# Performance work log

Hardware: AMD Instinct MI355X
Metric: run time of the kernel (lower is better)

Reference implementation:

```python
import jax, jax.numpy as jnp
import numpy as np

B, D_IN, D_OUT, N_CTRL = 8192, 512, 512, 8

def setup_inputs() -> dict:
    key = jax.random.key(0)
    k1, k2, k3, k4 = jax.random.split(key, 4)
    inputs = jax.random.normal(k1, (B, D_IN), dtype=jnp.float32)
    # routing weights: positive soft blend coefficients, normalized per sample
    raw = jax.random.uniform(k2, (B, N_CTRL), dtype=jnp.float32)
    weights = raw / jnp.sum(raw, axis=-1, keepdims=True)
    w = jax.random.normal(k3, (N_CTRL, D_IN, D_OUT), dtype=jnp.float32) * 0.05
    b = jax.random.normal(k4, (N_CTRL, D_OUT), dtype=jnp.float32) * 0.05
    return {"inputs": inputs, "weights": weights, "w": w, "b": b}

def reference(inputs, weights, w, b):
    # Original math: w_p = einsum('ji,imk->jmk', weights, w)  [B, D_IN, D_OUT]
    #                out = squeeze(inputs[:, None, :] @ w_p) + weights @ b
    # Fused equivalent avoiding the [B, D_IN, D_OUT] intermediate:
    # run all n_control expert matmuls, then blend by routing weights.
    per_expert = jnp.einsum('bi,cio->cbo', inputs, w)       # [C, B, D_OUT]
    out = jnp.einsum('bc,cbo->bo', weights, per_expert)     # [B, D_OUT]
    out = out + weights @ b                                 # blended bias [B, D_OUT]
    return out
```

## Files before the change

kernel.cpp:

```cpp
#include <hip/hip_runtime.h>

#define B_   8192
#define DIN  512
#define DOUT 512
#define NC   8
#define NCD  (NC * DIN)
#define KSPL 4

typedef float  f32x4 __attribute__((ext_vector_type(4)));
typedef short  s16x8 __attribute__((ext_vector_type(8)));
typedef unsigned short u16x4 __attribute__((ext_vector_type(4)));
typedef unsigned int   u32x4 __attribute__((ext_vector_type(4)));

__device__ __forceinline__ unsigned short f2bf(float f) {
  unsigned u = __builtin_bit_cast(unsigned, f);
  u += 0x7fffu + ((u >> 16) & 1u);
  return (unsigned short)(u >> 16);
}
__device__ __forceinline__ float bf2f(unsigned short h) {
  unsigned u = ((unsigned)h) << 16;
  return __builtin_bit_cast(float, u);
}
__device__ __forceinline__ unsigned cvtpk(float lo, float hi) {
  unsigned r;
  asm("v_cvt_pk_bf16_f32 %0, %1, %2" : "=v"(r) : "v"(lo), "v"(hi));
  return r;
}
__device__ __forceinline__ void gl2lds16(const void* g, void* l) {
  __builtin_amdgcn_global_load_lds(
      (const __attribute__((address_space(1))) void*)g,
      (__attribute__((address_space(3))) void*)l, 16, 0, 0);
}

__global__ void pack_xw_k(const f32x4* __restrict__ x, u16x4* __restrict__ xb,
                          const float* __restrict__ w, unsigned short* __restrict__ Wt) {
  __shared__ float tile[64][65];
  const int tid = threadIdx.x;
  if (blockIdx.x < 4096) {
    int gid = blockIdx.x * 256 + tid;
    f32x4 v = x[gid];
    u16x4 o;
    o[0] = f2bf(v[0]); o[1] = f2bf(v[1]); o[2] = f2bf(v[2]); o[3] = f2bf(v[3]);
    xb[gid] = o;
    return;
  }
  const int idx = blockIdx.x - 4096;
  const int kt = idx & 63, nt = idx >> 6;
#pragma unroll
  for (int it = 0; it < 16; ++it) {
    int u = it * 256 + tid;
    int r = u >> 6, cc = u & 63;
    tile[r][cc] = w[(size_t)(kt * 64 + r) * DOUT + nt * 64 + cc];
  }
  __syncthreads();
#pragma unroll
  for (int it = 0; it < 16; ++it) {
    int u = it * 256 + tid;
    int rn = u >> 6, ck = u & 63;
    Wt[(size_t)(nt * 64 + rn) * NCD + kt * 64 + ck] = f2bf(tile[ck][rn]);
  }
}

__global__ __launch_bounds__(512, 2) void gemm_k(
    const unsigned short* __restrict__ xb,
    const unsigned short* __restrict__ Wt,
    const float* __restrict__ wt,
    unsigned short* __restrict__ part) {
  extern __shared__ char smem[];
  const int tid  = threadIdx.x;
  const int lane = tid & 63, wid = tid >> 6;
  const int wm = wid >> 2, wn = wid & 3;
  const int l15 = lane & 15, lhi = lane >> 4;

  const int n0   = blockIdx.x;
  const int by   = n0 >> 3;
  const int bx   = (n0 >> 2) & 1;
  const int ks   = n0 & 3;
  const int brow = by * 256, bcol = bx * 256;

  const int srow = tid >> 3, schunk = tid & 7;
  const int swz  = schunk ^ (srow & 7);
  const unsigned short* gA = xb + (size_t)(brow + srow) * DIN + schunk * 8;
  const unsigned short* gB = Wt + (size_t)(bcol + srow) * NCD + ks * 1024 + swz * 8;
  char* adst = smem + srow * 128 + swz * 16;

  const float* wtp = wt + (size_t)(brow + srow) * NC + ks * 2;
  const float wtv0_0 = wtp[0],            wtv1_0 = wtp[1];
  const float wtv0_1 = wtp[64 * NC],      wtv1_1 = wtp[64 * NC + 1];
  const float wtv0_2 = wtp[128 * NC],     wtv1_2 = wtp[128 * NC + 1];
  const float wtv0_3 = wtp[192 * NC],     wtv1_3 = wtp[192 * NC + 1];

  f32x4 acc[8][4] = {};
  s16x8 areg0, areg1, areg2, areg3;
  s16x8 a[8], b[4];
  const int x7    = l15 & 7;
  const int pc0   = (lhi ^ x7) * 16;
  const int pc1   = ((4 + lhi) ^ x7) * 16;
  const int abase = (wm * 128 + l15) * 128;
  const int bbase = 32768 + (wn * 64 + l15) * 128;

#define STAGE_B(kt, ob) {                                                    \
    const unsigned short* s_ = gB + (size_t)(kt) * 64;                       \
    char* l_ = smem + (ob) + 32768 + tid * 16;                               \
    gl2lds16(s_,                          l_);                               \
    gl2lds16(s_ + (size_t) 64 * NCD,      l_ + 8192);                        \
    gl2lds16(s_ + (size_t)128 * NCD,      l_ + 16384);                       \
    gl2lds16(s_ + (size_t)192 * NCD,      l_ + 24576); }
#define LOAD_AREGS(kt) {                                                     \
    const unsigned short* s_ = gA + ((kt) & 7) * 64;                         \
    areg0 = *(const s16x8*)(s_);                                             \
    areg1 = *(const s16x8*)(s_ + (size_t) 64 * DIN);                         \
    areg2 = *(const s16x8*)(s_ + (size_t)128 * DIN);                         \
    areg3 = *(const s16x8*)(s_ + (size_t)192 * DIN); }
#define SCALE_STORE(AR, S, P, ob) {                                          \
    u32x4 v_;                                                                \
    v_[0] = cvtpk(bf2f((unsigned short)AR[0]) * (S),                         \
                  bf2f((unsigned short)AR[1]) * (S));                        \
    v_[1] = cvtpk(bf2f((unsigned short)AR[2]) * (S),                         \
                  bf2f((unsigned short)AR[3]) * (S));                        \
    v_[2] = cvtpk(bf2f((unsigned short)AR[4]) * (S),                         \
                  bf2f((unsigned short)AR[5]) * (S));                        \
    v_[3] = cvtpk(bf2f((unsigned short)AR[6]) * (S),                         \
                  bf2f((unsigned short)AR[7]) * (S));                        \
    *(u32x4*)(adst + (ob) + (P) * 8192) = v_; }
#define SCALE_WRITE_ALL(e_, ob) {                                            \
    SCALE_STORE(areg0, (e_) ? wtv1_0 : wtv0_0, 0, ob);                       \
    SCALE_STORE(areg1, (e_) ? wtv1_1 : wtv0_1, 1, ob);                       \
    SCALE_STORE(areg2, (e_) ? wtv1_2 : wtv0_2, 2, ob);                       \
    SCALE_STORE(areg3, (e_) ? wtv1_3 : wtv0_3, 3, ob); }
#define LOAD_FRAGS(cb, PC) {                                                 \
    const char* base_ = smem + (cb);                                         \
    _Pragma("unroll") for (int m = 0; m < 8; ++m)                            \
      a[m] = *(const s16x8*)(base_ + abase + m * 2048 + (PC));               \
    _Pragma("unroll") for (int n = 0; n < 4; ++n)                            \
      b[n] = *(const s16x8*)(base_ + bbase + n * 2048 + (PC)); }
#define MFMA_PAIR(N0, N1)                                                    \
    _Pragma("unroll") for (int m = 0; m < 8; ++m) {                          \
      acc[m][N0] = __builtin_amdgcn_mfma_f32_16x16x32_bf16(a[m], b[N0], acc[m][N0], 0, 0, 0); \
      acc[m][N1] = __builtin_amdgcn_mfma_f32_16x16x32_bf16(a[m], b[N1], acc[m][N1], 0, 0, 0); }
#define BAR()   __builtin_amdgcn_s_barrier()
#define PRIO1() __builtin_amdgcn_s_setprio(1)
#define PRIO0() __builtin_amdgcn_s_setprio(0)
#define PIN()   asm volatile("" ::: "memory")

  PIN();
  LOAD_AREGS(0);
  PIN();
  STAGE_B(0, 0);
  asm volatile("s_waitcnt vmcnt(4)" ::: "memory");
  SCALE_WRITE_ALL(0, 0);
  LOAD_AREGS(1);
  asm volatile("s_waitcnt lgkmcnt(0)" ::: "memory");

  for (int t = 0; t < 16; ++t) {
    const int cb = (t & 1) * 65536, ob = 65536 - cb;
    if (t < 15) {
      STAGE_B(t + 1, ob);
      asm volatile("s_waitcnt vmcnt(8)" ::: "memory");
    } else {
      asm volatile("s_waitcnt vmcnt(0)" ::: "memory");
    }
    BAR();
    LOAD_FRAGS(cb, pc0);
    PRIO1(); MFMA_PAIR(0, 1); MFMA_PAIR(2, 3); PRIO0();
    LOAD_FRAGS(cb, pc1);
    if (t < 15) {
      asm volatile("s_waitcnt vmcnt(4)" ::: "memory");
      const int e = ((t + 1) >> 3) & 1;
      SCALE_WRITE_ALL(e, ob);
      if (t < 14) LOAD_AREGS(t + 2);
    }
    asm volatile("s_waitcnt lgkmcnt(0)" ::: "memory");
    PRIO1(); MFMA_PAIR(0, 1); MFMA_PAIR(2, 3); PRIO0();
    BAR();
  }

  unsigned short* Cs = (unsigned short*)smem;
#pragma unroll
  for (int m = 0; m < 8; ++m)
#pragma unroll
    for (int n = 0; n < 4; ++n) {
      const int row = wm * 128 + m * 16 + lhi * 4;
      const int col = wn * 64 + n * 16 + l15;
      f32x4 v = acc[m][n];
#pragma unroll
      for (int j = 0; j < 4; ++j)
        Cs[(row + j) * 264 + col] = f2bf(v[j]);
    }
  __syncthreads();
  unsigned short* pc = part + (size_t)ks * (B_ * DOUT) + (size_t)brow * DOUT + bcol;
#pragma unroll
  for (int it = 0; it < 16; ++it) {
    const int u = it * 512 + tid;
    const int row = u >> 5, cu = (u & 31) * 8;
    f32x4 v = *(const f32x4*)(Cs + row * 264 + cu);
    *(f32x4*)(pc + (size_t)row * DOUT + cu) = v;
  }
#undef STAGE_B
#undef LOAD_AREGS
#undef SCALE_STORE
#undef SCALE_WRITE_ALL
#undef LOAD_FRAGS
#undef MFMA_PAIR
#undef BAR
#undef PRIO1
#undef PRIO0
#undef PIN
}

__global__ void reduce_k(const unsigned short* __restrict__ part,
                         const float* __restrict__ wt,
                         const float* __restrict__ bias,
                         float* __restrict__ out) {
  int gid = blockIdx.x * 256 + threadIdx.x;
  int b = gid >> 7;
  int o4 = (gid & 127) << 2;
  float w8[8];
  *(f32x4*)w8       = *(const f32x4*)(wt + (size_t)b * NC);
  *(f32x4*)(w8 + 4) = *(const f32x4*)(wt + (size_t)b * NC + 4);
  f32x4 acc = {0.f, 0.f, 0.f, 0.f};
  const size_t off = (size_t)b * DOUT + o4;
#pragma unroll
  for (int s = 0; s < KSPL; ++s) {
    u16x4 p = *(const u16x4*)(part + (size_t)s * (B_ * DOUT) + off);
#pragma unroll
    for (int i = 0; i < 4; ++i) acc[i] += bf2f(p[i]);
  }
#pragma unroll
  for (int cc = 0; cc < NC; ++cc) {
    f32x4 bi = *(const f32x4*)(bias + cc * DOUT + o4);
#pragma unroll
    for (int i = 0; i < 4; ++i) acc[i] += w8[cc] * bi[i];
  }
  *(f32x4*)(out + off) = acc;
}

__global__ void bias_only_k(const float* __restrict__ wt,
                            const float* __restrict__ bias,
                            float* __restrict__ out) {
  int gid = blockIdx.x * 256 + threadIdx.x;
  int b = gid >> 7;
  int o4 = (gid & 127) << 2;
  float w8[8];
  *(f32x4*)w8       = *(const f32x4*)(wt + (size_t)b * NC);
  *(f32x4*)(w8 + 4) = *(const f32x4*)(wt + (size_t)b * NC + 4);
  f32x4 acc = {0.f, 0.f, 0.f, 0.f};
#pragma unroll
  for (int cc = 0; cc < NC; ++cc) {
    f32x4 bi = *(const f32x4*)(bias + cc * DOUT + o4);
#pragma unroll
    for (int i = 0; i < 4; ++i) acc[i] += w8[cc] * bi[i];
  }
  *(f32x4*)(out + (size_t)b * DOUT + o4) = acc;
}

extern "C" void kernel_launch(void* const* d_in, const int* in_sizes, int n_in,
                              void* d_out, int out_size, void* d_ws, size_t ws_size,
                              hipStream_t stream) {
  const float *x = nullptr, *wtc = nullptr, *w = nullptr, *bias = nullptr;
  for (int i = 0; i < n_in; ++i) {
    switch (in_sizes[i]) {
      case B_ * DIN:        x    = (const float*)d_in[i]; break;
      case B_ * NC:         wtc  = (const float*)d_in[i]; break;
      case NC * DIN * DOUT: w    = (const float*)d_in[i]; break;
      case NC * DOUT:       bias = (const float*)d_in[i]; break;
    }
  }
  float* out = (float*)d_out;

  const size_t XB_ELEMS   = (size_t)B_ * DIN;
  const size_t WT_ELEMS   = (size_t)DOUT * NCD;
  const size_t PART_ELEMS = (size_t)KSPL * B_ * DOUT;
  const size_t need = (XB_ELEMS + WT_ELEMS + PART_ELEMS) * sizeof(unsigned short);

  if (ws_size < need) {
    bias_only_k<<<(B_ * DOUT / 4) / 256, 256, 0, stream>>>(wtc, bias, out);
    return;
  }

  unsigned short* xb   = (unsigned short*)d_ws;
  unsigned short* Wt   = xb + XB_ELEMS;
  unsigned short* part = Wt + WT_ELEMS;

  const int GEMM_LDS = 256 * 264 * 2;
  (void)hipFuncSetAttribute((const void*)gemm_k,
                            hipFuncAttributeMaxDynamicSharedMemorySize, GEMM_LDS);

  pack_xw_k<<<4096 + 512, 256, 0, stream>>>((const f32x4*)x, (u16x4*)xb, w, Wt);
  gemm_k<<<256, 512, GEMM_LDS, stream>>>(xb, Wt, wtc, part);
  reduce_k<<<(B_ * DOUT / 4) / 256, 256, 0, stream>>>(part, wtc, bias, out);
}
```

Before: 63.29 us.

## Interleave LDS fragment reads with quarter-sized MFMA groups and drop trailing barrier

Breaks each k-step's fragment loads and MFMAs into four quarters (4 A rows × 4 B cols), reading the next A/B fragments from LDS while the previous quarter's MFMAs run, which cuts register pressure for fragments. The B global-to-LDS staging for the next tile moves after the top barrier, and the end-of-iteration barrier is removed. A sched_barrier pins ordering, and a __syncthreads is added before the epilogue. The aim is better overlap of LDS reads and global loads with MFMA work and one fewer barrier per iteration, at the risk of tighter vmcnt accounting and possible races on the double-buffered LDS.

Measured after the change: 64.81 us. 1.02x slower.

```diff
diff --git a/kernel.cpp b/kernel.cpp
--- a/kernel.cpp
+++ b/kernel.cpp
@@ -92,7 +92,7 @@
 
   f32x4 acc[8][4] = {};
   s16x8 areg0, areg1, areg2, areg3;
-  s16x8 a[8], b[4];
+  s16x8 a[4], b0q[4], b1q[4];
   const int x7    = l15 & 7;
   const int pc0   = (lhi ^ x7) * 16;
   const int pc1   = ((4 + lhi) ^ x7) * 16;
@@ -128,16 +128,23 @@
     SCALE_STORE(areg1, (e_) ? wtv1_1 : wtv0_1, 1, ob);                       \
     SCALE_STORE(areg2, (e_) ? wtv1_2 : wtv0_2, 2, ob);                       \
     SCALE_STORE(areg3, (e_) ? wtv1_3 : wtv0_3, 3, ob); }
-#define LOAD_FRAGS(cb, PC) {                                                 \
-    const char* base_ = smem + (cb);                                         \
-    _Pragma("unroll") for (int m = 0; m < 8; ++m)                            \
-      a[m] = *(const s16x8*)(base_ + abase + m * 2048 + (PC));               \
-    _Pragma("unroll") for (int n = 0; n < 4; ++n)                            \
-      b[n] = *(const s16x8*)(base_ + bbase + n * 2048 + (PC)); }
-#define MFMA_PAIR(N0, N1)                                                    \
-    _Pragma("unroll") for (int m = 0; m < 8; ++m) {                          \
-      acc[m][N0] = __builtin_amdgcn_mfma_f32_16x16x32_bf16(a[m], b[N0], acc[m][N0], 0, 0, 0); \
-      acc[m][N1] = __builtin_amdgcn_mfma_f32_16x16x32_bf16(a[m], b[N1], acc[m][N1], 0, 0, 0); }
+#define RD_A(cbase, MOFF, PC) {                                              \
+    const char* p_ = smem + (cbase) + abase + (PC);                          \
+    a[0] = *(const s16x8*)(p_ + ((MOFF) + 0) * 2048);                        \
+    a[1] = *(const s16x8*)(p_ + ((MOFF) + 1) * 2048);                        \
+    a[2] = *(const s16x8*)(p_ + ((MOFF) + 2) * 2048);                        \
+    a[3] = *(const s16x8*)(p_ + ((MOFF) + 3) * 2048); }
+#define RD_B(cbase, PC, BQ) {                                                \
+    const char* p_ = smem + (cbase) + bbase + (PC);                          \
+    BQ[0] = *(const s16x8*)(p_);                                             \
+    BQ[1] = *(const s16x8*)(p_ + 2048);                                      \
+    BQ[2] = *(const s16x8*)(p_ + 4096);                                      \
+    BQ[3] = *(const s16x8*)(p_ + 6144); }
+#define MFMA_Q(MOFF, BQ)                                                     \
+    _Pragma("unroll") for (int j = 0; j < 4; ++j)                            \
+      _Pragma("unroll") for (int n = 0; n < 4; ++n)                          \
+        acc[(MOFF) + j][n] = __builtin_amdgcn_mfma_f32_16x16x32_bf16(        \
+            a[j], BQ[n], acc[(MOFF) + j][n], 0, 0, 0);
 #define BAR()   __builtin_amdgcn_s_barrier()
 #define PRIO1() __builtin_amdgcn_s_setprio(1)
 #define PRIO0() __builtin_amdgcn_s_setprio(0)
@@ -155,26 +162,31 @@
   for (int t = 0; t < 16; ++t) {
     const int cb = (t & 1) * 65536, ob = 65536 - cb;
     if (t < 15) {
-      STAGE_B(t + 1, ob);
-      asm volatile("s_waitcnt vmcnt(8)" ::: "memory");
+      asm volatile("s_waitcnt vmcnt(4)" ::: "memory");
     } else {
       asm volatile("s_waitcnt vmcnt(0)" ::: "memory");
     }
     BAR();
-    LOAD_FRAGS(cb, pc0);
-    PRIO1(); MFMA_PAIR(0, 1); MFMA_PAIR(2, 3); PRIO0();
-    LOAD_FRAGS(cb, pc1);
+    if (t < 15) STAGE_B(t + 1, ob);
+    RD_A(cb, 0, pc0); RD_B(cb, pc0, b0q);
+    PRIO1(); MFMA_Q(0, b0q); PRIO0();
+    RD_A(cb, 4, pc0); RD_B(cb, pc1, b1q);
+    PRIO1(); MFMA_Q(4, b0q); PRIO0();
+    RD_A(cb, 0, pc1);
     if (t < 15) {
       asm volatile("s_waitcnt vmcnt(4)" ::: "memory");
       const int e = ((t + 1) >> 3) & 1;
       SCALE_WRITE_ALL(e, ob);
-      if (t < 14) LOAD_AREGS(t + 2);
     }
+    PRIO1(); MFMA_Q(0, b1q); PRIO0();
+    RD_A(cb, 4, pc1);
+    if (t < 14) LOAD_AREGS(t + 2);
     asm volatile("s_waitcnt lgkmcnt(0)" ::: "memory");
-    PRIO1(); MFMA_PAIR(0, 1); MFMA_PAIR(2, 3); PRIO0();
-    BAR();
-  }
-
+    __builtin_amdgcn_sched_barrier(0);
+    PRIO1(); MFMA_Q(4, b1q); PRIO0();
+  }
+
+  __syncthreads();
   unsigned short* Cs = (unsigned short*)smem;
 #pragma unroll
   for (int m = 0; m < 8; ++m)
@@ -200,8 +212,9 @@
 #undef LOAD_AREGS
 #undef SCALE_STORE
 #undef SCALE_WRITE_ALL
-#undef LOAD_FRAGS
-#undef MFMA_PAIR
+#undef RD_A
+#undef RD_B
+#undef MFMA_Q
 #undef BAR
 #undef PRIO1
 #undef PRIO0
```

## Split K-tiles into half-step B ring buffer with 4-way swizzle layout

Applied to the files above, without the earlier changes.

Restructures the LDS layout so each 64-wide K tile is stored as two 32-wide halves with a 4-way XOR swizzle. B is streamed through a four-slot ring of half-tiles, while A keeps a double buffer. Each loop iteration now issues one B half-stage per MFMA half, with a barrier before each half and explicit sched_barriers. The goal is finer-grained overlap of global-to-LDS loads with MFMA work and lower LDS footprint per stage. The cost is an extra barrier per iteration, and the changed swizzle may alter LDS bank-conflict behaviour.

Measured after the change: 65.11 us. 1.03x slower.

```diff
diff --git a/kernel.cpp b/kernel.cpp
--- a/kernel.cpp
+++ b/kernel.cpp
@@ -79,10 +79,13 @@
   const int brow = by * 256, bcol = bx * 256;
 
   const int srow = tid >> 3, schunk = tid & 7;
-  const int swz  = schunk ^ (srow & 7);
   const unsigned short* gA = xb + (size_t)(brow + srow) * DIN + schunk * 8;
-  const unsigned short* gB = Wt + (size_t)(bcol + srow) * NCD + ks * 1024 + swz * 8;
-  char* adst = smem + srow * 128 + swz * 16;
+  const int adst_off = (schunk >> 2) * 16384 + srow * 64
+                     + (((schunk & 3) ^ (srow & 3)) << 4);
+
+  const int br = tid >> 2, bc = tid & 3;
+  const unsigned short* gB0 = Wt + (size_t)(bcol + br) * NCD + ks * 1024
+                                 + ((bc ^ (br & 3)) * 8);
 
   const float* wtp = wt + (size_t)(brow + srow) * NC + ks * 2;
   const float wtv0_0 = wtp[0],            wtv1_0 = wtp[1];
@@ -93,26 +96,22 @@
   f32x4 acc[8][4] = {};
   s16x8 areg0, areg1, areg2, areg3;
   s16x8 a[8], b[4];
-  const int x7    = l15 & 7;
-  const int pc0   = (lhi ^ x7) * 16;
-  const int pc1   = ((4 + lhi) ^ x7) * 16;
-  const int abase = (wm * 128 + l15) * 128;
-  const int bbase = 32768 + (wn * 64 + l15) * 128;
-
-#define STAGE_B(kt, ob) {                                                    \
-    const unsigned short* s_ = gB + (size_t)(kt) * 64;                       \
-    char* l_ = smem + (ob) + 32768 + tid * 16;                               \
-    gl2lds16(s_,                          l_);                               \
-    gl2lds16(s_ + (size_t) 64 * NCD,      l_ + 8192);                        \
-    gl2lds16(s_ + (size_t)128 * NCD,      l_ + 16384);                       \
-    gl2lds16(s_ + (size_t)192 * NCD,      l_ + 24576); }
+  const int key    = (lhi ^ (l15 & 3)) << 4;
+  const int abase2 = (wm * 128 + l15) * 64 + key;
+  const int bbase2 = (wn * 64  + l15) * 64 + key;
+
+#define STAGE_BH(H) {                                                        \
+    const unsigned short* s_ = gB0 + ((H) >> 1) * 64 + ((H) & 1) * 32;       \
+    char* l_ = smem + 65536 + ((H) & 3) * 16384 + tid * 16;                  \
+    gl2lds16(s_, l_);                                                        \
+    gl2lds16(s_ + (size_t)128 * NCD, l_ + 8192); }
 #define LOAD_AREGS(kt) {                                                     \
     const unsigned short* s_ = gA + ((kt) & 7) * 64;                         \
     areg0 = *(const s16x8*)(s_);                                             \
     areg1 = *(const s16x8*)(s_ + (size_t) 64 * DIN);                         \
     areg2 = *(const s16x8*)(s_ + (size_t)128 * DIN);                         \
     areg3 = *(const s16x8*)(s_ + (size_t)192 * DIN); }
-#define SCALE_STORE(AR, S, P, ob) {                                          \
+#define SCALE_STORE(AR, S, P, slotb) {                                       \
     u32x4 v_;                                                                \
     v_[0] = cvtpk(bf2f((unsigned short)AR[0]) * (S),                         \
                   bf2f((unsigned short)AR[1]) * (S));                        \
@@ -122,65 +121,71 @@
                   bf2f((unsigned short)AR[5]) * (S));                        \
     v_[3] = cvtpk(bf2f((unsigned short)AR[6]) * (S),                         \
                   bf2f((unsigned short)AR[7]) * (S));                        \
-    *(u32x4*)(adst + (ob) + (P) * 8192) = v_; }
-#define SCALE_WRITE_ALL(e_, ob) {                                            \
-    SCALE_STORE(areg0, (e_) ? wtv1_0 : wtv0_0, 0, ob);                       \
-    SCALE_STORE(areg1, (e_) ? wtv1_1 : wtv0_1, 1, ob);                       \
-    SCALE_STORE(areg2, (e_) ? wtv1_2 : wtv0_2, 2, ob);                       \
-    SCALE_STORE(areg3, (e_) ? wtv1_3 : wtv0_3, 3, ob); }
-#define LOAD_FRAGS(cb, PC) {                                                 \
-    const char* base_ = smem + (cb);                                         \
+    *(u32x4*)(smem + (slotb) + adst_off + (P) * 4096) = v_; }
+#define SCALE_WRITE_ALL(e_, slotb) {                                         \
+    SCALE_STORE(areg0, (e_) ? wtv1_0 : wtv0_0, 0, slotb);                    \
+    SCALE_STORE(areg1, (e_) ? wtv1_1 : wtv0_1, 1, slotb);                    \
+    SCALE_STORE(areg2, (e_) ? wtv1_2 : wtv0_2, 2, slotb);                    \
+    SCALE_STORE(areg3, (e_) ? wtv1_3 : wtv0_3, 3, slotb); }
+#define RD_HALF(aslotb, kk, bslot) {                                         \
+    const char* pa_ = smem + (aslotb) + (kk) * 16384 + abase2;               \
+    const char* pb_ = smem + 65536 + (bslot) * 16384 + bbase2;               \
     _Pragma("unroll") for (int m = 0; m < 8; ++m)                            \
-      a[m] = *(const s16x8*)(base_ + abase + m * 2048 + (PC));               \
+      a[m] = *(const s16x8*)(pa_ + m * 1024);                                \
     _Pragma("unroll") for (int n = 0; n < 4; ++n)                            \
-      b[n] = *(const s16x8*)(base_ + bbase + n * 2048 + (PC)); }
-#define MFMA_PAIR(N0, N1)                                                    \
-    _Pragma("unroll") for (int m = 0; m < 8; ++m) {                          \
-      acc[m][N0] = __builtin_amdgcn_mfma_f32_16x16x32_bf16(a[m], b[N0], acc[m][N0], 0, 0, 0); \
-      acc[m][N1] = __builtin_amdgcn_mfma_f32_16x16x32_bf16(a[m], b[N1], acc[m][N1], 0, 0, 0); }
+      b[n] = *(const s16x8*)(pb_ + n * 1024); }
+#define MFMA_HALF()                                                          \
+    _Pragma("unroll") for (int m = 0; m < 8; ++m)                            \
+      _Pragma("unroll") for (int n = 0; n < 4; ++n)                          \
+        acc[m][n] = __builtin_amdgcn_mfma_f32_16x16x32_bf16(                 \
+            a[m], b[n], acc[m][n], 0, 0, 0);
 #define BAR()   __builtin_amdgcn_s_barrier()
 #define PRIO1() __builtin_amdgcn_s_setprio(1)
 #define PRIO0() __builtin_amdgcn_s_setprio(0)
 #define PIN()   asm volatile("" ::: "memory")
+#define WAITV(N) asm volatile("s_waitcnt vmcnt(" #N ")" ::: "memory")
+#define WAITL()  asm volatile("s_waitcnt lgkmcnt(0)" ::: "memory")
 
   PIN();
   LOAD_AREGS(0);
   PIN();
-  STAGE_B(0, 0);
-  asm volatile("s_waitcnt vmcnt(4)" ::: "memory");
+  STAGE_BH(0); STAGE_BH(1);
+  WAITV(4);
   SCALE_WRITE_ALL(0, 0);
   LOAD_AREGS(1);
-  asm volatile("s_waitcnt lgkmcnt(0)" ::: "memory");
+  WAITL();
 
   for (int t = 0; t < 16; ++t) {
-    const int cb = (t & 1) * 65536, ob = 65536 - cb;
+    const int aslot = (t & 1) * 32768, oslot = 32768 - aslot;
+    if (t < 15) { STAGE_BH(2 * t + 2); WAITV(8); }
+    else        { WAITV(2); }
+    BAR(); PIN();
+    RD_HALF(aslot, 0, (2 * t) & 3);
+    WAITL();
+    __builtin_amdgcn_sched_barrier(0);
+    PRIO1(); MFMA_HALF(); PRIO0();
+    if (t < 15) { STAGE_BH(2 * t + 3); WAITV(8); }
+    else        { WAITV(0); }
+    BAR(); PIN();
+    RD_HALF(aslot, 1, (2 * t + 1) & 3);
     if (t < 15) {
-      STAGE_B(t + 1, ob);
-      asm volatile("s_waitcnt vmcnt(8)" ::: "memory");
-    } else {
-      asm volatile("s_waitcnt vmcnt(0)" ::: "memory");
-    }
-    BAR();
-    LOAD_FRAGS(cb, pc0);
-    PRIO1(); MFMA_PAIR(0, 1); MFMA_PAIR(2, 3); PRIO0();
-    LOAD_FRAGS(cb, pc1);
-    if (t < 15) {
-      asm volatile("s_waitcnt vmcnt(4)" ::: "memory");
-      const int e = ((t + 1) >> 3) & 1;
-      SCALE_WRITE_ALL(e, ob);
+      WAITV(4);
+      const int e = (t + 1) >> 3;
+      SCALE_WRITE_ALL(e, oslot);
       if (t < 14) LOAD_AREGS(t + 2);
     }
-    asm volatile("s_waitcnt lgkmcnt(0)" ::: "memory");
-    PRIO1(); MFMA_PAIR(0, 1); MFMA_PAIR(2, 3); PRIO0();
-    BAR();
-  }
-
+    WAITL();
+    __builtin_amdgcn_sched_barrier(0);
+    PRIO1(); MFMA_HALF(); PRIO0();
+  }
+
+  __syncthreads();
   unsigned short* Cs = (unsigned short*)smem;
 #pragma unroll
   for (int m = 0; m < 8; ++m)
 #pragma unroll
     for (int n = 0; n < 4; ++n) {
-      const int row = wm * 128 + m * 16 + lhi * 4;
+      const int row = wm * 128 + m * 16 + (lane >> 4) * 4;
       const int col = wn * 64 + n * 16 + l15;
       f32x4 v = acc[m][n];
 #pragma unroll
@@ -196,16 +201,18 @@
     f32x4 v = *(const f32x4*)(Cs + row * 264 + cu);
     *(f32x4*)(pc + (size_t)row * DOUT + cu) = v;
   }
-#undef STAGE_B
+#undef STAGE_BH
 #undef LOAD_AREGS
 #undef SCALE_STORE
 #undef SCALE_WRITE_ALL
-#undef LOAD_FRAGS
-#undef MFMA_PAIR
+#undef RD_HALF
+#undef MFMA_HALF
 #undef BAR
 #undef PRIO1
 #undef PRIO0
 #undef PIN
+#undef WAITV
+#undef WAITL
 }
 
 __global__ void reduce_k(const unsigned short* __restrict__ part,
```
